# Performance work log

Measured on AMD Instinct MI355X. Metric: run time of the kernel, lower is better.

## Reference

```python
import jax, jax.numpy as jnp
import numpy as np

EPS = 1e-8


def box2corners(box):
    # box: (B, N, 5) = (x, y, w, h, angle_rad) -> corners (B, N, 4, 2)
    x, y, w, h, a = (box[..., i] for i in range(5))
    xs = jnp.array([0.5, -0.5, -0.5, 0.5], box.dtype) * w[..., None]
    ys = jnp.array([0.5, 0.5, -0.5, -0.5], box.dtype) * h[..., None]
    cos, sin = jnp.cos(a)[..., None], jnp.sin(a)[..., None]
    cx = xs * cos - ys * sin + x[..., None]
    cy = xs * sin + ys * cos + y[..., None]
    return jnp.stack([cx, cy], axis=-1)


def edge_intersections(c1, c2):
    # all 4x4 edge-pair segment intersections -> pts (B,N,16,2), mask (B,N,16)
    p = c1[..., :, None, :]                                  # (B,N,4,1,2)
    r = (jnp.roll(c1, -1, axis=-2) - c1)[..., :, None, :]     # edge dirs of box1
    q = c2[..., None, :, :]                                  # (B,N,1,4,2)
    s = (jnp.roll(c2, -1, axis=-2) - c2)[..., None, :, :]     # edge dirs of box2
    qp = q - p
    rxs = r[..., 0] * s[..., 1] - r[..., 1] * s[..., 0]
    t = (qp[..., 0] * s[..., 1] - qp[..., 1] * s[..., 0]) / (rxs + EPS)
    u = (qp[..., 0] * r[..., 1] - qp[..., 1] * r[..., 0]) / (rxs + EPS)
    mask = (t > 0.) & (t < 1.) & (u > 0.) & (u < 1.)
    pts = (p + t[..., None] * r) * mask[..., None]
    B, N = c1.shape[0], c1.shape[1]
    return pts.reshape(B, N, 16, 2), mask.reshape(B, N, 16)


def box_in_box(corners1, corners2):
    # True where corners of box1 lie inside box2 -> (B,N,4)
    a = corners2[..., 0:1, :]
    b = corners2[..., 1:2, :]
    d = corners2[..., 3:4, :]
    ab, ad, am = b - a, d - a, corners1 - a
    p_ab = jnp.sum(ab * am, -1) / (jnp.sum(ab * ab, -1) + EPS)
    p_ad = jnp.sum(ad * am, -1) / (jnp.sum(ad * ad, -1) + EPS)
    tol = 1e-6
    return (p_ab > -tol) & (p_ab < 1. + tol) & (p_ad > -tol) & (p_ad < 1. + tol)


def convex_area(verts, mask):
    # shoelace area of valid vertices, sorted CCW by angle around their mean
    m = mask.astype(verts.dtype)
    nv = jnp.sum(m, axis=-1)                                          # (B,N)
    mean = jnp.sum(verts * m[..., None], axis=-2) / jnp.maximum(nv, 1.)[..., None]
    v = verts - mean[..., None, :]
    ang = jnp.where(mask, jnp.arctan2(v[..., 1], v[..., 0]), 1e9)      # invalid sort last
    order = jnp.argsort(ang, axis=-1)
    v_s = jnp.take_along_axis(v, order[..., None], axis=-2)
    m_s = jnp.take_along_axis(mask, order, axis=-1)
    v_s = jnp.where(m_s[..., None], v_s, v_s[..., 0:1, :])  # pad tail with first vertex -> zero cross terms
    v_n = jnp.roll(v_s, -1, axis=-2)
    cross = v_s[..., 0] * v_n[..., 1] - v_s[..., 1] * v_n[..., 0]
    area = 0.5 * jnp.abs(jnp.sum(cross, axis=-1))
    return jnp.where(nv >= 3., area, 0.)


def diff_iou_rotated_2d(box1, box2):
    c1, c2 = box2corners(box1), box2corners(box2)
    pts, m_int = edge_intersections(c1, c2)
    m1 = box_in_box(c1, c2)
    m2 = box_in_box(c2, c1)
    verts = jnp.concatenate([c1, c2, pts], axis=-2)    # (B,N,24,2)
    mask = jnp.concatenate([m1, m2, m_int], axis=-1)   # (B,N,24)
    inter = convex_area(verts, mask)
    area1 = box1[..., 2] * box1[..., 3]
    area2 = box2[..., 2] * box2[..., 3]
    union = area1 + area2 - inter
    return inter / (union + EPS)


def setup_inputs() -> dict:
    key = jax.random.key(0)
    k1, k2, k3 = jax.random.split(key, 3)
    B, A, W, H = 16, 3, 128, 128
    pred = jax.random.uniform(k1, (B, A, W, H, 5), dtype=jnp.float32)
    target = jax.random.uniform(k2, (B, A, W, H, 5), dtype=jnp.float32)
    pos_idx = jax.random.randint(k3, (B, A, W, H), 0, 2).astype(bool)
    return {"pred": pred, "target": target, "pos_idx": pos_idx}


def reference(pred, target, pos_idx):
    eps = 1e-7
    target = target.at[..., -1].set(jnp.deg2rad(target[..., -1] * 180. - 180.))
    pred = pred.at[..., -1].set(jnp.deg2rad(pred[..., -1]))
    bs, A, w, h = target.shape[:-1]
    ious = diff_iou_rotated_2d(pred.reshape(1, -1, 5), target.reshape(1, -1, 5))
    ious = jnp.clip(ious.reshape(bs, A, w, h), eps, 1. - eps)
    m = pos_idx.astype(ious.dtype)
    # mode == 'linear': loss = 1 - iou, mean over positive samples
    loss = jnp.sum((1. - ious) * m) / jnp.maximum(jnp.sum(m), 1.)
    return loss, ious
```

## Files before the change

kernel.cpp:

```cpp
#include <hip/hip_runtime.h>

#define FEPS 1e-8f

__device__ __forceinline__ void clip_edge_accum(
    float px, float py, float dx, float dy,
    float cx, float cy, float ux, float uy,
    float hw, float hh, float& sum)
{
    float rx = px - cx, ry = py - cy;
    float a0 = rx * ux + ry * uy;
    float b0 = dx * ux + dy * uy;
    float a1 = -rx * uy + ry * ux;
    float b1 = -dx * uy + dy * ux;

    float t0 = 0.0f, t1 = 1.0f;
    bool reject = false;
    {
        bool par = fabsf(b0) < 1e-12f;
        float inv = 1.0f / (par ? 1.0f : b0);
        float tA = (hw - a0) * inv, tB = (-hw - a0) * inv;
        t0 = par ? t0 : fmaxf(t0, fminf(tA, tB));
        t1 = par ? t1 : fminf(t1, fmaxf(tA, tB));
        reject = reject || (par && (fabsf(a0) > hw));
    }
    {
        bool par = fabsf(b1) < 1e-12f;
        float inv = 1.0f / (par ? 1.0f : b1);
        float tA = (hh - a1) * inv, tB = (-hh - a1) * inv;
        t0 = par ? t0 : fmaxf(t0, fminf(tA, tB));
        t1 = par ? t1 : fminf(t1, fmaxf(tA, tB));
        reject = reject || (par && (fabsf(a1) > hh));
    }
    bool ok = (!reject) && (t1 > t0);
    float sx = px + t0 * dx, sy = py + t0 * dy;
    float ex = px + t1 * dx, ey = py + t1 * dy;
    sum += ok ? (sx * ey - ex * sy) : 0.0f;
}

__device__ __forceinline__ float one_iou(
    float p0, float p1, float p2, float p3, float p4,
    float t0, float t1, float t2, float t3, float t4)
{
    const float DEG = 0.017453292519943295f;
    float a1 = p4 * DEG;
    float a2 = (t4 * 180.0f - 180.0f) * DEG;
    float s1 = __sinf(a1), c1_ = __cosf(a1);
    float s2 = __sinf(a2), c2_ = __cosf(a2);

    float hw1 = 0.5f * p2, hh1 = 0.5f * p3;
    float hw2 = 0.5f * t2, hh2 = 0.5f * t3;

    const float SX[4] = {0.5f, -0.5f, -0.5f, 0.5f};
    const float SY[4] = {0.5f, 0.5f, -0.5f, -0.5f};
    float P1x[4], P1y[4], P2x[4], P2y[4];
    #pragma unroll
    for (int k = 0; k < 4; ++k) {
        float xs = SX[k] * p2, ys = SY[k] * p3;
        P1x[k] = xs * c1_ - ys * s1 + p0;
        P1y[k] = xs * s1 + ys * c1_ + p1;
        float xs2 = SX[k] * t2, ys2 = SY[k] * t3;
        P2x[k] = xs2 * c2_ - ys2 * s2 + t0;
        P2y[k] = xs2 * s2 + ys2 * c2_ + t1;
    }

    float sum = 0.0f;
    #pragma unroll
    for (int k = 0; k < 4; ++k) {
        int kn = (k + 1) & 3;
        clip_edge_accum(P1x[k], P1y[k], P1x[kn]-P1x[k], P1y[kn]-P1y[k],
                        t0, t1, c2_, s2, hw2, hh2, sum);
    }
    #pragma unroll
    for (int k = 0; k < 4; ++k) {
        int kn = (k + 1) & 3;
        clip_edge_accum(P2x[k], P2y[k], P2x[kn]-P2x[k], P2y[kn]-P2y[k],
                        p0, p1, c1_, s1, hw1, hh1, sum);
    }

    float inter = 0.5f * fabsf(sum);
    float uni = p2 * p3 + t2 * t3 - inter;
    float iou = inter / (uni + FEPS);
    return fminf(fmaxf(iou, 1e-7f), 1.0f - 1e-7f);
}

__global__ __launch_bounds__(256) void riou_kernel(
    const float* __restrict__ pred, const float* __restrict__ target,
    const int* __restrict__ pos_idx, float* __restrict__ out,
    float2* __restrict__ partials, int n)
{
    int gid = blockIdx.x * blockDim.x + threadIdx.x;
    float lnum = 0.0f, lden = 0.0f;

    if (gid < n) {
        const float* p = pred + (size_t)gid * 5;
        const float* t = target + (size_t)gid * 5;
        float iou = one_iou(p[0], p[1], p[2], p[3], p[4],
                            t[0], t[1], t[2], t[3], t[4]);
        out[1 + gid] = iou;
        float m = (pos_idx[gid] != 0) ? 1.0f : 0.0f;
        lnum = (1.0f - iou) * m;
        lden = m;
    }

    #pragma unroll
    for (int off = 32; off > 0; off >>= 1) {
        lnum += __shfl_down(lnum, off);
        lden += __shfl_down(lden, off);
    }
    __shared__ float snum[4], sden[4];
    int wave = threadIdx.x >> 6, lane = threadIdx.x & 63;
    if (lane == 0) { snum[wave] = lnum; sden[wave] = lden; }
    __syncthreads();
    if (threadIdx.x == 0) {
        float bn = snum[0] + snum[1] + snum[2] + snum[3];
        float bd = sden[0] + sden[1] + sden[2] + sden[3];
        partials[blockIdx.x] = make_float2(bn, bd);
    }
}

__global__ __launch_bounds__(256) void riou_finalize(
    const float2* __restrict__ partials, int nb, float* __restrict__ out)
{
    double num = 0.0, den = 0.0;
    for (int i = threadIdx.x; i < nb; i += 256) {
        float2 p = partials[i];
        num += (double)p.x;
        den += (double)p.y;
    }
    #pragma unroll
    for (int off = 32; off > 0; off >>= 1) {
        num += __shfl_down(num, off);
        den += __shfl_down(den, off);
    }
    __shared__ double dn[4], dd[4];
    int wave = threadIdx.x >> 6, lane = threadIdx.x & 63;
    if (lane == 0) { dn[wave] = num; dd[wave] = den; }
    __syncthreads();
    if (threadIdx.x == 0) {
        double n2 = dn[0] + dn[1] + dn[2] + dn[3];
        double d2 = dd[0] + dd[1] + dd[2] + dd[3];
        out[0] = (float)(n2 / fmax(d2, 1.0));
    }
}

extern "C" void kernel_launch(void* const* d_in, const int* in_sizes, int n_in,
                              void* d_out, int out_size, void* d_ws, size_t ws_size,
                              hipStream_t stream) {
    const float* pred   = (const float*)d_in[0];
    const float* target = (const float*)d_in[1];
    const int*   posidx = (const int*)d_in[2];
    float* out = (float*)d_out;

    int n = in_sizes[0] / 5;

    int block = 256;
    int grid = (n + block - 1) / block;
    float2* partials = (float2*)d_ws;

    riou_kernel<<<grid, block, 0, stream>>>(pred, target, posidx, out,
                                            partials, n);
    riou_finalize<<<1, block, 0, stream>>>(partials, grid, out);
}
```

Before: 94.16 us.

## Fuse finalize into main kernel via slotted atomics and last-block reduction

Replaces the separate finalize launch with per-block atomic accumulation into 64 padded slots plus a completion counter, and the last-finishing block reduces the slots and writes the loss. A memset of the workspace is added before the launch, and launch bounds now request 4 blocks per SM. This is meant to remove the second kernel launch and its serial pass over the partials, at the cost of atomic contention, a threadfence, and float-order nondeterminism in the final sum.

```diff
diff --git a/kernel.cpp b/kernel.cpp
--- a/kernel.cpp
+++ b/kernel.cpp
@@ -1,6 +1,8 @@
 #include <hip/hip_runtime.h>
 
 #define FEPS 1e-8f
+#define NSLOTS 64
+#define SLOT_STRIDE 64
 
 __device__ __forceinline__ void clip_edge_accum(
     float px, float py, float dx, float dy,
@@ -83,10 +85,10 @@
     return fminf(fmaxf(iou, 1e-7f), 1.0f - 1e-7f);
 }
 
-__global__ __launch_bounds__(256) void riou_kernel(
+__global__ __launch_bounds__(256, 4) void riou_fused(
     const float* __restrict__ pred, const float* __restrict__ target,
     const int* __restrict__ pos_idx, float* __restrict__ out,
-    float2* __restrict__ partials, int n)
+    char* __restrict__ ws, int n, int nblocks)
 {
     int gid = blockIdx.x * blockDim.x + threadIdx.x;
     float lnum = 0.0f, lden = 0.0f;
@@ -108,38 +110,39 @@
         lden += __shfl_down(lden, off);
     }
     __shared__ float snum[4], sden[4];
+    __shared__ int slast;
     int wave = threadIdx.x >> 6, lane = threadIdx.x & 63;
     if (lane == 0) { snum[wave] = lnum; sden[wave] = lden; }
     __syncthreads();
+
     if (threadIdx.x == 0) {
         float bn = snum[0] + snum[1] + snum[2] + snum[3];
         float bd = sden[0] + sden[1] + sden[2] + sden[3];
-        partials[blockIdx.x] = make_float2(bn, bd);
+        char* slot = ws + (size_t)(blockIdx.x & (NSLOTS - 1)) * SLOT_STRIDE;
+        atomicAdd((float*)slot, bn);
+        atomicAdd((float*)(slot + 4), bd);
+        __threadfence();
+        unsigned t = atomicAdd((unsigned*)(ws + NSLOTS * SLOT_STRIDE), 1u);
+        slast = (t == (unsigned)(nblocks - 1)) ? 1 : 0;
     }
-}
+    __syncthreads();
 
-__global__ __launch_bounds__(256) void riou_finalize(
-    const float2* __restrict__ partials, int nb, float* __restrict__ out)
-{
-    double num = 0.0, den = 0.0;
-    for (int i = threadIdx.x; i < nb; i += 256) {
-        float2 p = partials[i];
-        num += (double)p.x;
-        den += (double)p.y;
-    }
-    #pragma unroll
-    for (int off = 32; off > 0; off >>= 1) {
-        num += __shfl_down(num, off);
-        den += __shfl_down(den, off);
-    }
-    __shared__ double dn[4], dd[4];
-    int wave = threadIdx.x >> 6, lane = threadIdx.x & 63;
-    if (lane == 0) { dn[wave] = num; dd[wave] = den; }
-    __syncthreads();
-    if (threadIdx.x == 0) {
-        double n2 = dn[0] + dn[1] + dn[2] + dn[3];
-        double d2 = dd[0] + dd[1] + dd[2] + dd[3];
-        out[0] = (float)(n2 / fmax(d2, 1.0));
+    if (slast) {
+        float num = 0.0f, den = 0.0f;
+        if (threadIdx.x < NSLOTS) {
+            char* slot = ws + (size_t)threadIdx.x * SLOT_STRIDE;
+            num = atomicAdd((float*)slot, 0.0f);
+            den = atomicAdd((float*)(slot + 4), 0.0f);
+        }
+        if (threadIdx.x < 64) {
+            #pragma unroll
+            for (int off = 32; off > 0; off >>= 1) {
+                num += __shfl_down(num, off);
+                den += __shfl_down(den, off);
+            }
+            if (threadIdx.x == 0)
+                out[0] = num / fmaxf(den, 1.0f);
+        }
     }
 }
 
@@ -152,12 +155,11 @@
     float* out = (float*)d_out;
 
     int n = in_sizes[0] / 5;
-
     int block = 256;
     int grid = (n + block - 1) / block;
-    float2* partials = (float2*)d_ws;
 
-    riou_kernel<<<grid, block, 0, stream>>>(pred, target, posidx, out,
-                                            partials, n);
-    riou_finalize<<<1, block, 0, stream>>>(partials, grid, out);
+    hipMemsetAsync(d_ws, 0, NSLOTS * SLOT_STRIDE + 64, stream);
+
+    riou_fused<<<grid, block, 0, stream>>>(pred, target, posidx, out,
+                                           (char*)d_ws, n, grid);
 }
```

Result: slower. 153.2 us (+62.7%).
